# Optimization experiments

Measured on AMD Instinct MI355X. Metric: run time of the kernel, lower is better.

The kernel has to match this reference:

```python
import jax, jax.numpy as jnp
import numpy as np

B, N, T, D, H, E = 32768, 2, 4, 256, 8, 2
HD = D // H
S = N * T  # flattened seq_len = num_nodes * history_length
SCALE = 1.0 / np.sqrt(HD)


def setup_inputs() -> dict:
    key = jax.random.key(0)
    ks = jax.random.split(key, 22)

    def w(k, i, o):
        return jax.random.normal(k, (i, o), jnp.float32) * 0.02

    def b(k, o):
        return jax.random.normal(k, (o,), jnp.float32) * 0.01

    return {
        'node_features': jax.random.normal(ks[0], (B, N, T, D), jnp.float32),
        'edge_features': jax.random.normal(ks[1], (B, E), jnp.float32),
        'Wq': w(ks[2], D, D), 'bq': b(ks[3], D),
        'Wk': w(ks[4], D, D), 'bk': b(ks[5], D),
        'Wv': w(ks[6], D, D), 'bv': b(ks[7], D),
        'Wo': w(ks[8], D, D), 'bo': b(ks[9], D),
        'Wbias': w(ks[10], E, H), 'bbias': b(ks[11], H),
        'Wgate': w(ks[12], E, D), 'bgate': b(ks[13], D),
        'Wscale': w(ks[14], E, D), 'bscale': b(ks[15], D),
        'Wshift': w(ks[16], E, D), 'bshift': b(ks[17], D),
        'Whs': w(ks[18], E, H), 'bhs': b(ks[19], H),
    }


def reference(node_features, edge_features, Wq, bq, Wk, bk, Wv, bv, Wo, bo,
              Wbias, bbias, Wgate, bgate, Wscale, bscale, Wshift, bshift, Whs, bhs):
    # temporal mode: [B, N, T, D] -> [B, S, D]
    x = node_features.reshape(B, S, D)
    e = edge_features  # [B, E]

    Q = x @ Wq + bq
    K = x @ Wk + bk
    V = x @ Wv + bv

    # Edge-Conditioned Modulation of V
    gate = jax.nn.sigmoid(e @ Wgate + bgate)   # [B, D]
    scale = jnp.tanh(e @ Wscale + bscale)       # [B, D]
    shift = e @ Wshift + bshift                 # [B, D]
    V = (V * (1.0 + scale[:, None, :]) + shift[:, None, :]) * gate[:, None, :]

    # [B, H, S, HD]
    Qh = Q.reshape(B, S, H, HD).transpose(0, 2, 1, 3)
    Kh = K.reshape(B, S, H, HD).transpose(0, 2, 1, 3)
    Vh = V.reshape(B, S, H, HD).transpose(0, 2, 1, 3)

    scores = jnp.einsum('bhsd,bhtd->bhst', Qh, Kh) * SCALE  # [B, H, S, S]

    edge_bias = e @ Wbias + bbias                 # [B, H]
    head_scale = jnp.tanh(e @ Whs + bhs)          # [B, H]
    scores = scores * (1.0 + head_scale[:, :, None, None])

    # sparse temporal bias: (ee_t, obj_t) and (obj_t, ee_t) pairs only
    ee = jnp.arange(T)
    obj = T + ee
    bias = jnp.zeros((B, H, S, S), scores.dtype)
    bias = bias.at[:, :, ee, obj].set(edge_bias[:, :, None])
    bias = bias.at[:, :, obj, ee].set(edge_bias[:, :, None])
    scores = scores + bias

    attn = jax.nn.softmax(scores, axis=-1)  # dropout is identity in eval
    out = jnp.einsum('bhst,bhtd->bhsd', attn, Vh)  # [B, H, S, HD]
    out = out.transpose(0, 2, 1, 3).reshape(B, N, T, D).mean(axis=2)  # temporal pooling
    out = out @ Wo + bo  # [B, N, D]
    return out
```

## Files before the change

### kernel.cpp

```cpp
#include <hip/hip_runtime.h>


typedef short bf16x8 __attribute__((ext_vector_type(8)));
typedef float f32x4 __attribute__((ext_vector_type(4)));
typedef unsigned short u16;

#define SCALE_F 0.17677669529663687f
#define WT_BYTES (1024 * 256 * 2)

__device__ __forceinline__ float bf2f(u16 h) {
  unsigned u = ((unsigned)h) << 16; float f; __builtin_memcpy(&f, &u, 4); return f;
}
__device__ __forceinline__ u16 f2bf(float f) {
  unsigned u; __builtin_memcpy(&u, &f, 4);
  u += 0x7FFFu + ((u >> 16) & 1u);
  return (u16)(u >> 16);
}
__device__ __forceinline__ float fast_tanh(float x) {
  float e = __expf(2.0f * x);
  return (e - 1.0f) / (e + 1.0f);
}

template<bool F32>
__device__ __forceinline__ float LD(const void* p, int i) {
  if constexpr (F32) return ((const float*)p)[i];
  else return bf2f(((const u16*)p)[i]);
}

template<bool F32>
__device__ __forceinline__ bf16x8 load8bf(const void* p, int idx) {
  if constexpr (F32) {
    const float* f = (const float*)p + idx;
    float4 a = *(const float4*)f;
    float4 b = *(const float4*)(f + 4);
    bf16x8 r;
    r[0] = (short)f2bf(a.x); r[1] = (short)f2bf(a.y);
    r[2] = (short)f2bf(a.z); r[3] = (short)f2bf(a.w);
    r[4] = (short)f2bf(b.x); r[5] = (short)f2bf(b.y);
    r[6] = (short)f2bf(b.z); r[7] = (short)f2bf(b.w);
    return r;
  } else {
    return *(const bf16x8*)((const u16*)p + idx);
  }
}

__device__ __forceinline__ void gl_lds16(const u16* g, u16* l) {
  __builtin_amdgcn_global_load_lds(
      (const __attribute__((address_space(1))) unsigned int*)g,
      (__attribute__((address_space(3))) unsigned int*)l, 16, 0, 0);
}

__global__ void prep_kernel(const u16* __restrict__ x16,
                            const void* __restrict__ Wq, const void* __restrict__ Wk,
                            const void* __restrict__ Wv, const void* __restrict__ Wo,
                            int* __restrict__ flag, u16* __restrict__ WT) {
  __shared__ int tot;
  if (threadIdx.x == 0) tot = 0;
  __syncthreads();
  int cnt = 0;
  for (int i = threadIdx.x; i < 4096; i += 256) {
    int e = (x16[2 * i] >> 7) & 0xFF;
    cnt += (e >= 0x90 || e <= 0x50) ? 1 : 0;
  }
  atomicAdd(&tot, cnt);
  __syncthreads();
  const bool f32 = (tot >= 64);
  if (blockIdx.x == 0 && threadIdx.x == 0) *flag = f32 ? 1 : 0;

  int n = blockIdx.x;
  int k = threadIdx.x;
  if (n < 768) {
    int sel = n >> 8, col = n & 255;
    const void* src = sel == 0 ? Wq : (sel == 1 ? Wk : Wv);
    float v = f32 ? ((const float*)src)[k * 256 + col] : bf2f(((const u16*)src)[k * 256 + col]);
    WT[n * 256 + (k ^ ((n & 7) << 3))] = f2bf(v);
  } else {
    int col = n - 768;
    float v = f32 ? ((const float*)Wo)[k * 256 + col] : bf2f(((const u16*)Wo)[k * 256 + col]);
    WT[768 * 256 + col * 256 + k] = f2bf(v);
  }
}

struct __align__(16) Scratch {
  u16 qk[4][32][72];
  u16 vt[4][32][56];
  u16 pb[4][16][40];
};
union SharedU {
  u16 wtile[3 * 32 * 128];
  Scratch s;
};

template<bool F32>
__device__ __forceinline__ void fused_impl(
    SharedU& sm,
    const void* __restrict__ x, const void* __restrict__ edge,
    const void* __restrict__ bq, const void* __restrict__ bk, const void* __restrict__ bv,
    const void* __restrict__ Wbias, const void* __restrict__ bbias,
    const void* __restrict__ Wgate, const void* __restrict__ bgate,
    const void* __restrict__ Wscale, const void* __restrict__ bscale,
    const void* __restrict__ Wshift, const void* __restrict__ bshift,
    const void* __restrict__ Whs, const void* __restrict__ bhs,
    const u16* __restrict__ WT, float* __restrict__ out) {
  const int tid = threadIdx.x;
  const int w  = tid >> 6;
  const int l  = tid & 63;
  const int ln = l & 15;
  const int q4 = l >> 4;
  u16* poolg = (u16*)out;

  {
    u16* vz = &sm.s.vt[w][0][0];
#pragma unroll
    for (int i = 0; i < 28; ++i) vz[l + 64 * i] = 0;
    u16* pz = &sm.s.pb[w][0][0];
#pragma unroll
    for (int i = 0; i < 10; ++i) pz[l + 64 * i] = 0;
  }

  float eA[4], eB[4];
#pragma unroll
  for (int i = 0; i < 4; ++i) {
    int gb = blockIdx.x * 16 + w * 4 + i;
    eA[i] = LD<F32>(edge, gb * 2);
    eB[i] = LD<F32>(edge, gb * 2 + 1);
  }

  const int xbase = (blockIdx.x * 128 + w * 32) * 256;
  bf16x8 xa[2][8];
#pragma unroll
  for (int mt = 0; mt < 2; ++mt)
#pragma unroll
    for (int ks = 0; ks < 8; ++ks)
      xa[mt][ks] = load8bf<F32>(x, xbase + (mt * 16 + ln) * 256 + ks * 32 + q4 * 8);

  int rowoff[6];
#pragma unroll
  for (int nt = 0; nt < 6; ++nt)
    rowoff[nt] = ((nt >> 1) * 32 + (nt & 1) * 16 + ln) * 128;
  const int swz = (ln & 7) << 3;

#pragma unroll 1
  for (int h = 0; h < 8; ++h) {
    f32x4 acc[2][6];
#pragma unroll
    for (int mt = 0; mt < 2; ++mt)
#pragma unroll
      for (int nt = 0; nt < 6; ++nt) acc[mt][nt] = (f32x4){0.f, 0.f, 0.f, 0.f};

#pragma unroll
    for (int half = 0; half < 2; ++half) {
      __syncthreads();
#pragma unroll
      for (int i = 0; i < 6; ++i) {
        int el = i * 2048 + tid * 8;
        int r = el >> 7, c = el & 127;
        int ng = ((r >> 5) << 8) + h * 32 + (r & 31);
        gl_lds16(WT + ng * 256 + half * 128 + c,
                 sm.wtile + i * 2048 + w * 512);
      }
      __syncthreads();
#pragma unroll
      for (int k2 = 0; k2 < 4; ++k2) {
        int cx = (k2 * 32 + q4 * 8) ^ swz;
#pragma unroll
        for (int nt = 0; nt < 6; ++nt) {
          bf16x8 bfr = *(const bf16x8*)(sm.wtile + rowoff[nt] + cx);
          acc[0][nt] = __builtin_amdgcn_mfma_f32_16x16x32_bf16(xa[0][half * 4 + k2], bfr, acc[0][nt], 0, 0, 0);
          acc[1][nt] = __builtin_amdgcn_mfma_f32_16x16x32_bf16(xa[1][half * 4 + k2], bfr, acc[1][nt], 0, 0, 0);
        }
      }
    }
    __syncthreads();

#pragma unroll
    for (int nt = 0; nt < 4; ++nt) {
      int cb = (nt & 1) * 16 + ln;
      float bias = LD<F32>((nt >> 1) ? bk : bq, h * 32 + cb);
      int col = (nt >> 1) * 32 + cb;
#pragma unroll
      for (int mt = 0; mt < 2; ++mt)
#pragma unroll
        for (int r = 0; r < 4; ++r)
          sm.s.qk[w][mt * 16 + q4 * 4 + r][col] = f2bf(acc[mt][nt][r] + bias);
    }
#pragma unroll
    for (int nt = 4; nt < 6; ++nt) {
      int dg = h * 32 + (nt - 4) * 16 + ln;
      float bvv = LD<F32>(bv, dg);
      float wg0 = LD<F32>(Wgate, dg),  wg1 = LD<F32>(Wgate, 256 + dg),  bg  = LD<F32>(bgate, dg);
      float ws0 = LD<F32>(Wscale, dg), ws1 = LD<F32>(Wscale, 256 + dg), bs  = LD<F32>(bscale, dg);
      float wf0 = LD<F32>(Wshift, dg), wf1 = LD<F32>(Wshift, 256 + dg), bsh = LD<F32>(bshift, dg);
#pragma unroll
      for (int mt = 0; mt < 2; ++mt) {
        float e0 = (q4 & 2) ? eA[mt * 2 + 1] : eA[mt * 2];
        float e1 = (q4 & 2) ? eB[mt * 2 + 1] : eB[mt * 2];
        float ga = 1.f / (1.f + __expf(-(e0 * wg0 + e1 * wg1 + bg)));
        float sc = fast_tanh(e0 * ws0 + e1 * ws1 + bs);
        float sh = e0 * wf0 + e1 * wf1 + bsh;
        u16 vv[4];
#pragma unroll
        for (int r = 0; r < 4; ++r) {
          float v = acc[mt][nt][r] + bvv;
          v = (v * (1.f + sc) + sh) * ga;
          vv[r] = f2bf(v);
        }
        ushort4 pk; pk.x = vv[0]; pk.y = vv[1]; pk.z = vv[2]; pk.w = vv[3];
        *(ushort4*)&sm.s.vt[w][(nt - 4) * 16 + ln][mt * 16 + q4 * 4] = pk;
      }
    }
    __asm__ volatile("" ::: "memory");

    float wb0 = LD<F32>(Wbias, h), wb1 = LD<F32>(Wbias, 8 + h), bb  = LD<F32>(bbias, h);
    float wh0 = LD<F32>(Whs, h),   wh1 = LD<F32>(Whs, 8 + h),   bh_ = LD<F32>(bhs, h);
#pragma unroll
    for (int pair = 0; pair < 2; ++pair) {
      bf16x8 qa = *(const bf16x8*)&sm.s.qk[w][pair * 16 + ln][q4 * 8];
      bf16x8 kb = *(const bf16x8*)&sm.s.qk[w][pair * 16 + ln][32 + q4 * 8];
      f32x4 z4 = {0.f, 0.f, 0.f, 0.f};
      f32x4 s = __builtin_amdgcn_mfma_f32_16x16x32_bf16(qa, kb, z4, 0, 0, 0);

      float e00 = eA[pair * 2],     e01 = eB[pair * 2];
      float e10 = eA[pair * 2 + 1], e11 = eB[pair * 2 + 1];
      float eb0 = e00 * wb0 + e01 * wb1 + bb;
      float eb1 = e10 * wb0 + e11 * wb1 + bb;
      float hs0 = fast_tanh(e00 * wh0 + e01 * wh1 + bh_);
      float hs1 = fast_tanh(e10 * wh0 + e11 * wh1 + bh_);
      int bj = ln >> 3;
      float mult = SCALE_F * (1.f + (bj ? hs1 : hs0));
      float ebias = bj ? eb1 : eb0;
      int tl = ln & 7;
      bool valid = ((q4 >> 1) == bj);
      float p[4];
#pragma unroll
      for (int r = 0; r < 4; ++r) {
        int sl = (q4 & 1) * 4 + r;
        p[r] = s[r] * mult + ((tl == (sl ^ 4)) ? ebias : 0.f);
      }
#pragma unroll
      for (int r = 0; r < 4; ++r) {
        float m = p[r];
        m = fmaxf(m, __shfl_xor(m, 1));
        m = fmaxf(m, __shfl_xor(m, 2));
        m = fmaxf(m, __shfl_xor(m, 4));
        float e = __expf(p[r] - m);
        float su = e;
        su += __shfl_xor(su, 1);
        su += __shfl_xor(su, 2);
        su += __shfl_xor(su, 4);
        p[r] = e / su;
      }
#pragma unroll
      for (int r = 0; r < 4; ++r)
        sm.s.pb[w][q4 * 4 + r][ln] = valid ? f2bf(p[r]) : (u16)0;
      __asm__ volatile("" ::: "memory");

      bf16x8 pa = *(const bf16x8*)&sm.s.pb[w][ln][q4 * 8];
#pragma unroll
      for (int nt = 0; nt < 2; ++nt) {
        bf16x8 vb = *(const bf16x8*)&sm.s.vt[w][nt * 16 + ln][pair * 16 + q4 * 8];
        f32x4 z = {0.f, 0.f, 0.f, 0.f};
        f32x4 o = __builtin_amdgcn_mfma_f32_16x16x32_bf16(pa, vb, z, 0, 0, 0);
        float pm = (o[0] + o[1] + o[2] + o[3]) * 0.25f;
        int prow = w * 8 + (pair * 2 + (q4 >> 1)) * 2 + (q4 & 1);
        poolg[(blockIdx.x * 32 + prow) * 512 + 256 + h * 32 + nt * 16 + ln] = f2bf(pm);
      }
    }
  }
}

__global__ __launch_bounds__(256, 4) void fused_kernel(
    const void* __restrict__ x, const void* __restrict__ edge,
    const void* __restrict__ bq, const void* __restrict__ bk, const void* __restrict__ bv,
    const void* __restrict__ Wbias, const void* __restrict__ bbias,
    const void* __restrict__ Wgate, const void* __restrict__ bgate,
    const void* __restrict__ Wscale, const void* __restrict__ bscale,
    const void* __restrict__ Wshift, const void* __restrict__ bshift,
    const void* __restrict__ Whs, const void* __restrict__ bhs,
    const int* __restrict__ flag, const u16* __restrict__ WT, float* __restrict__ out) {
  __shared__ SharedU sm;
  if (*flag)
    fused_impl<true>(sm, x, edge, bq, bk, bv, Wbias, bbias, Wgate, bgate,
                     Wscale, bscale, Wshift, bshift, Whs, bhs, WT, out);
  else
    fused_impl<false>(sm, x, edge, bq, bk, bv, Wbias, bbias, Wgate, bgate,
                      Wscale, bscale, Wshift, bshift, Whs, bhs, WT, out);
}

template<bool F32>
__device__ __forceinline__ void proj_impl(const void* __restrict__ bo,
                                          const u16* __restrict__ WT,
                                          float* __restrict__ out) {
  const int tid = threadIdx.x;
  const int w  = tid >> 6;
  const int l  = tid & 63;
  const int ln = l & 15;
  const int q4 = l >> 4;
  const u16* pool = (const u16*)out;
  const u16* WoT = WT + 768 * 256;
  const int rbase = blockIdx.x * 32;

  f32x4 fo[2][4];
#pragma unroll
  for (int mt = 0; mt < 2; ++mt)
#pragma unroll
    for (int nt = 0; nt < 4; ++nt) fo[mt][nt] = (f32x4){0.f, 0.f, 0.f, 0.f};
#pragma unroll
  for (int ks = 0; ks < 8; ++ks) {
    bf16x8 af0 = *(const bf16x8*)(pool + (rbase + ln) * 512 + 256 + ks * 32 + q4 * 8);
    bf16x8 af1 = *(const bf16x8*)(pool + (rbase + 16 + ln) * 512 + 256 + ks * 32 + q4 * 8);
#pragma unroll
    for (int ntw = 0; ntw < 4; ++ntw) {
      int nrow = w * 64 + ntw * 16 + ln;
      bf16x8 bfr = *(const bf16x8*)(WoT + nrow * 256 + ks * 32 + q4 * 8);
      fo[0][ntw] = __builtin_amdgcn_mfma_f32_16x16x32_bf16(af0, bfr, fo[0][ntw], 0, 0, 0);
      fo[1][ntw] = __builtin_amdgcn_mfma_f32_16x16x32_bf16(af1, bfr, fo[1][ntw], 0, 0, 0);
    }
  }
  __syncthreads();
#pragma unroll
  for (int ntw = 0; ntw < 4; ++ntw) {
    int col = w * 64 + ntw * 16 + ln;
    float bias = LD<F32>(bo, col);
#pragma unroll
    for (int mt = 0; mt < 2; ++mt)
#pragma unroll
      for (int r = 0; r < 4; ++r) {
        int row = mt * 16 + q4 * 4 + r;
        out[(rbase + row) * 256 + col] = fo[mt][ntw][r] + bias;
      }
  }
}

__global__ __launch_bounds__(256, 4) void proj_kernel(const void* __restrict__ bo,
                                                      const int* __restrict__ flag,
                                                      const u16* __restrict__ WT,
                                                      float* __restrict__ out) {
  if (*flag) proj_impl<true>(bo, WT, out);
  else       proj_impl<false>(bo, WT, out);
}

extern "C" void kernel_launch(void* const* d_in, const int* in_sizes, int n_in,
                              void* d_out, int out_size, void* d_ws, size_t ws_size,
                              hipStream_t stream) {
  (void)in_sizes; (void)n_in; (void)out_size; (void)ws_size;
  const void* x      = d_in[0];
  const void* edge   = d_in[1];
  const void* Wq     = d_in[2];  const void* bq  = d_in[3];
  const void* Wk     = d_in[4];  const void* bk  = d_in[5];
  const void* Wv     = d_in[6];  const void* bv  = d_in[7];
  const void* Wo     = d_in[8];  const void* bo  = d_in[9];
  const void* Wbias  = d_in[10]; const void* bbias  = d_in[11];
  const void* Wgate  = d_in[12]; const void* bgate  = d_in[13];
  const void* Wscale = d_in[14]; const void* bscale = d_in[15];
  const void* Wshift = d_in[16]; const void* bshift = d_in[17];
  const void* Whs    = d_in[18]; const void* bhs    = d_in[19];
  u16* WT   = (u16*)d_ws;
  int* flag = (int*)((char*)d_ws + WT_BYTES);
  float* out = (float*)d_out;

  prep_kernel<<<1024, 256, 0, stream>>>((const u16*)x, Wq, Wk, Wv, Wo, flag, WT);
  fused_kernel<<<2048, 256, 0, stream>>>(x, edge, bq, bk, bv, Wbias, bbias,
                                         Wgate, bgate, Wscale, bscale, Wshift, bshift,
                                         Whs, bhs, flag, WT, out);
  proj_kernel<<<2048, 256, 0, stream>>>(bo, flag, WT, out);
}
```

Baseline: 750.0 us.

## Double-buffer weight tiles in QKV GEMM and coalesce pooled intermediate writes

Splits each head's K dimension into four 64-wide chunks and double-buffers the weight tiles in LDS, so the global-to-LDS load of the next chunk overlaps the MFMAs on the current one. The per-chunk barriers replace the two large load/compute phases. Pooled attention outputs are now written in a lane-contiguous layout for coalesced stores, and the projection kernel restages them through shared memory to recover the row layout. Input x loads and final output stores become nontemporal. The cost is an extra LDS staging pass in the projection kernel and more barriers in the main loop.

```diff
diff --git a/kernel.cpp b/kernel.cpp
--- a/kernel.cpp
+++ b/kernel.cpp
@@ -28,19 +28,19 @@
 }
 
 template<bool F32>
-__device__ __forceinline__ bf16x8 load8bf(const void* p, int idx) {
+__device__ __forceinline__ bf16x8 load8bf_nt(const void* p, int idx) {
   if constexpr (F32) {
-    const float* f = (const float*)p + idx;
-    float4 a = *(const float4*)f;
-    float4 b = *(const float4*)(f + 4);
+    const f32x4* f = (const f32x4*)((const float*)p + idx);
+    f32x4 a = __builtin_nontemporal_load(f);
+    f32x4 b = __builtin_nontemporal_load(f + 1);
     bf16x8 r;
-    r[0] = (short)f2bf(a.x); r[1] = (short)f2bf(a.y);
-    r[2] = (short)f2bf(a.z); r[3] = (short)f2bf(a.w);
-    r[4] = (short)f2bf(b.x); r[5] = (short)f2bf(b.y);
-    r[6] = (short)f2bf(b.z); r[7] = (short)f2bf(b.w);
+    r[0] = (short)f2bf(a[0]); r[1] = (short)f2bf(a[1]);
+    r[2] = (short)f2bf(a[2]); r[3] = (short)f2bf(a[3]);
+    r[4] = (short)f2bf(b[0]); r[5] = (short)f2bf(b[1]);
+    r[6] = (short)f2bf(b[2]); r[7] = (short)f2bf(b[3]);
     return r;
   } else {
-    return *(const bf16x8*)((const u16*)p + idx);
+    return __builtin_nontemporal_load((const bf16x8*)((const u16*)p + idx));
   }
 }
 
@@ -87,7 +87,7 @@
   u16 pb[4][16][40];
 };
 union SharedU {
-  u16 wtile[3 * 32 * 128];
+  u16 wtile[2][6144];
   Scratch s;
 };
 
@@ -132,12 +132,19 @@
   for (int mt = 0; mt < 2; ++mt)
 #pragma unroll
     for (int ks = 0; ks < 8; ++ks)
-      xa[mt][ks] = load8bf<F32>(x, xbase + (mt * 16 + ln) * 256 + ks * 32 + q4 * 8);
-
+      xa[mt][ks] = load8bf_nt<F32>(x, xbase + (mt * 16 + ln) * 256 + ks * 32 + q4 * 8);
+
+  const u16* wsrc[3];
+#pragma unroll
+  for (int i = 0; i < 3; ++i) {
+    int r = i * 32 + w * 8 + (l >> 3);
+    int ngb = ((r >> 5) << 8) + (r & 31);
+    wsrc[i] = WT + ngb * 256 + (l & 7) * 8;
+  }
   int rowoff[6];
 #pragma unroll
   for (int nt = 0; nt < 6; ++nt)
-    rowoff[nt] = ((nt >> 1) * 32 + (nt & 1) * 16 + ln) * 128;
+    rowoff[nt] = ((nt >> 1) * 32 + (nt & 1) * 16 + ln) * 64;
   const int swz = (ln & 7) << 3;
 
 #pragma unroll 1
@@ -148,30 +155,32 @@
 #pragma unroll
       for (int nt = 0; nt < 6; ++nt) acc[mt][nt] = (f32x4){0.f, 0.f, 0.f, 0.f};
 
-#pragma unroll
-    for (int half = 0; half < 2; ++half) {
+    __syncthreads();
+#pragma unroll
+    for (int i = 0; i < 3; ++i)
+      gl_lds16(wsrc[i] + h * 8192, &sm.wtile[0][(i * 32 + w * 8) * 64]);
+    __syncthreads();
+#pragma unroll
+    for (int q = 0; q < 4; ++q) {
+      if (q < 3) {
+#pragma unroll
+        for (int i = 0; i < 3; ++i)
+          gl_lds16(wsrc[i] + h * 8192 + (q + 1) * 64,
+                   &sm.wtile[(q + 1) & 1][(i * 32 + w * 8) * 64]);
+      }
+#pragma unroll
+      for (int k2 = 0; k2 < 2; ++k2) {
+        int cx = (k2 * 32 + q4 * 8) ^ swz;
+        const u16* wq = &sm.wtile[q & 1][0];
+#pragma unroll
+        for (int nt = 0; nt < 6; ++nt) {
+          bf16x8 bfr = *(const bf16x8*)(wq + rowoff[nt] + cx);
+          acc[0][nt] = __builtin_amdgcn_mfma_f32_16x16x32_bf16(xa[0][q * 2 + k2], bfr, acc[0][nt], 0, 0, 0);
+          acc[1][nt] = __builtin_amdgcn_mfma_f32_16x16x32_bf16(xa[1][q * 2 + k2], bfr, acc[1][nt], 0, 0, 0);
+        }
+      }
       __syncthreads();
-#pragma unroll
-      for (int i = 0; i < 6; ++i) {
-        int el = i * 2048 + tid * 8;
-        int r = el >> 7, c = el & 127;
-        int ng = ((r >> 5) << 8) + h * 32 + (r & 31);
-        gl_lds16(WT + ng * 256 + half * 128 + c,
-                 sm.wtile + i * 2048 + w * 512);
-      }
-      __syncthreads();
-#pragma unroll
-      for (int k2 = 0; k2 < 4; ++k2) {
-        int cx = (k2 * 32 + q4 * 8) ^ swz;
-#pragma unroll
-        for (int nt = 0; nt < 6; ++nt) {
-          bf16x8 bfr = *(const bf16x8*)(sm.wtile + rowoff[nt] + cx);
-          acc[0][nt] = __builtin_amdgcn_mfma_f32_16x16x32_bf16(xa[0][half * 4 + k2], bfr, acc[0][nt], 0, 0, 0);
-          acc[1][nt] = __builtin_amdgcn_mfma_f32_16x16x32_bf16(xa[1][half * 4 + k2], bfr, acc[1][nt], 0, 0, 0);
-        }
-      }
-    }
-    __syncthreads();
+    }
 
 #pragma unroll
     for (int nt = 0; nt < 4; ++nt) {
@@ -262,8 +271,8 @@
         f32x4 z = {0.f, 0.f, 0.f, 0.f};
         f32x4 o = __builtin_amdgcn_mfma_f32_16x16x32_bf16(pa, vb, z, 0, 0, 0);
         float pm = (o[0] + o[1] + o[2] + o[3]) * 0.25f;
-        int prow = w * 8 + (pair * 2 + (q4 >> 1)) * 2 + (q4 & 1);
-        poolg[(blockIdx.x * 32 + prow) * 512 + 256 + h * 32 + nt * 16 + ln] = f2bf(pm);
+        int c = w * 32 + h * 4 + pair * 2 + nt;
+        poolg[(blockIdx.x * 32 + (c >> 2)) * 512 + 256 + (c & 3) * 64 + l] = f2bf(pm);
       }
     }
   }
@@ -287,10 +296,12 @@
                       Wscale, bscale, Wshift, bshift, Whs, bhs, WT, out);
 }
 
-template<bool F32>
-__device__ __forceinline__ void proj_impl(const void* __restrict__ bo,
-                                          const u16* __restrict__ WT,
-                                          float* __restrict__ out) {
+__global__ __launch_bounds__(256, 4) void proj_kernel(const void* __restrict__ bo,
+                                                      const int* __restrict__ flag,
+                                                      const u16* __restrict__ WT,
+                                                      float* __restrict__ out) {
+  __shared__ u16 pooled[32][264];
+  const bool f32 = (*flag != 0);
   const int tid = threadIdx.x;
   const int w  = tid >> 6;
   const int l  = tid & 63;
@@ -300,6 +311,18 @@
   const u16* WoT = WT + 768 * 256;
   const int rbase = blockIdx.x * 32;
 
+#pragma unroll
+  for (int i = 0; i < 32; ++i) {
+    int idx = i * 256 + tid;
+    int c = idx >> 6, lq = idx & 63;
+    u16 v = pool[(rbase + (c >> 2)) * 512 + 256 + (c & 3) * 64 + lq];
+    int wsrc = c >> 5, hh = (c >> 2) & 7, pr = (c >> 1) & 1, ntt = c & 1;
+    int q4l = lq >> 4, lnl = lq & 15;
+    int prow = wsrc * 8 + (pr * 2 + (q4l >> 1)) * 2 + (q4l & 1);
+    pooled[prow][hh * 32 + ntt * 16 + lnl] = v;
+  }
+  __syncthreads();
+
   f32x4 fo[2][4];
 #pragma unroll
   for (int mt = 0; mt < 2; ++mt)
@@ -307,8 +330,8 @@
     for (int nt = 0; nt < 4; ++nt) fo[mt][nt] = (f32x4){0.f, 0.f, 0.f, 0.f};
 #pragma unroll
   for (int ks = 0; ks < 8; ++ks) {
-    bf16x8 af0 = *(const bf16x8*)(pool + (rbase + ln) * 512 + 256 + ks * 32 + q4 * 8);
-    bf16x8 af1 = *(const bf16x8*)(pool + (rbase + 16 + ln) * 512 + 256 + ks * 32 + q4 * 8);
+    bf16x8 af0 = *(const bf16x8*)&pooled[ln][ks * 32 + q4 * 8];
+    bf16x8 af1 = *(const bf16x8*)&pooled[16 + ln][ks * 32 + q4 * 8];
 #pragma unroll
     for (int ntw = 0; ntw < 4; ++ntw) {
       int nrow = w * 64 + ntw * 16 + ln;
@@ -317,27 +340,19 @@
       fo[1][ntw] = __builtin_amdgcn_mfma_f32_16x16x32_bf16(af1, bfr, fo[1][ntw], 0, 0, 0);
     }
   }
-  __syncthreads();
 #pragma unroll
   for (int ntw = 0; ntw < 4; ++ntw) {
     int col = w * 64 + ntw * 16 + ln;
-    float bias = LD<F32>(bo, col);
+    float bias = f32 ? ((const float*)bo)[col] : bf2f(((const u16*)bo)[col]);
 #pragma unroll
     for (int mt = 0; mt < 2; ++mt)
 #pragma unroll
       for (int r = 0; r < 4; ++r) {
         int row = mt * 16 + q4 * 4 + r;
-        out[(rbase + row) * 256 + col] = fo[mt][ntw][r] + bias;
-      }
-  }
-}
-
-__global__ __launch_bounds__(256, 4) void proj_kernel(const void* __restrict__ bo,
-                                                      const int* __restrict__ flag,
-                                                      const u16* __restrict__ WT,
-                                                      float* __restrict__ out) {
-  if (*flag) proj_impl<true>(bo, WT, out);
-  else       proj_impl<false>(bo, WT, out);
+        __builtin_nontemporal_store(fo[mt][ntw][r] + bias,
+                                    &out[(rbase + row) * 256 + col]);
+      }
+  }
 }
 
 extern "C" void kernel_launch(void* const* d_in, const int* in_sizes, int n_in,
```

After: 736.3 us. About the same (-1.8%).
